# Kernel tuning notes

Hardware: AMD Instinct MI355X
Metric: run time of the kernel (lower is better)

Reference implementation:

```python
import jax, jax.numpy as jnp
import numpy as np
from jax import lax

B, C, IMG, P = 64, 3, 256, 16
D, K, NC, NH = 128, 512, 8, 4
GRID = IMG // P
N = GRID * GRID  # 256 patches
HD = D // NH


def setup_inputs() -> dict:
    key = jax.random.key(0)
    ks = jax.random.split(key, 16)
    s = 0.02
    f32 = jnp.float32
    return {
        'image': jax.random.uniform(ks[0], (B, C, IMG, IMG), f32),
        'conv_w': jax.random.normal(ks[1], (D, C, P, P), f32) * s,
        'conv_b': jnp.zeros((D,), f32),
        'stat_w1': jax.random.normal(ks[2], (128, 15), f32) * s,
        'stat_b1': jnp.zeros((128,), f32),
        'stat_w2': jax.random.normal(ks[3], (D, 128), f32) * s,
        'stat_b2': jnp.zeros((D,), f32),
        'pos_embed': jax.random.normal(ks[4], (1, N, D), f32) * s,
        'ln1_s': jnp.ones((2, D), f32), 'ln1_b': jnp.zeros((2, D), f32),
        'qkv_w': jax.random.normal(ks[5], (2, 3 * D, D), f32) * s,
        'qkv_b': jnp.zeros((2, 3 * D), f32),
        'out_w': jax.random.normal(ks[6], (2, D, D), f32) * s,
        'out_b': jnp.zeros((2, D), f32),
        'ln2_s': jnp.ones((2, D), f32), 'ln2_b': jnp.zeros((2, D), f32),
        'ff1_w': jax.random.normal(ks[7], (2, 2 * D, D), f32) * s,
        'ff1_b': jnp.zeros((2, 2 * D), f32),
        'ff2_w': jax.random.normal(ks[8], (2, D, 2 * D), f32) * s,
        'ff2_b': jnp.zeros((2, D), f32),
        'codebook': jax.random.uniform(ks[9], (K, D), f32, -1.0 / K, 1.0 / K),
        'head_w': jax.random.normal(ks[10], (NC, D), f32) * s,
        'head_b': jnp.zeros((NC,), f32),
    }


def _ln(x, s, b, eps=1e-5):
    mu = x.mean(-1, keepdims=True)
    var = jnp.var(x, axis=-1, keepdims=True)
    return (x - mu) / jnp.sqrt(var + eps) * s + b


def _stats(image):
    # mean/std(unbiased)/min/max per channel + skew/kurt/dark of luminance -> 15 feats
    px = image.reshape(B, C, -1)
    mean = px.mean(-1)
    std = px.std(-1, ddof=1)
    mn = px.min(-1)
    mx = px.max(-1)
    lum = 0.299 * px[:, 0] + 0.587 * px[:, 1] + 0.114 * px[:, 2]
    cen = lum - lum.mean(-1, keepdims=True)
    sd = lum.std(-1)  # biased, matches unbiased=False
    skew = (cen ** 3).mean(-1) / (sd ** 3 + 1e-6)
    kurt = (cen ** 4).mean(-1) / (sd ** 4 + 1e-6)
    dark = (lum < 0.2).astype(jnp.float32).mean(-1)
    return jnp.concatenate([mean, std, mn, mx, skew[:, None], kurt[:, None], dark[:, None]], -1)


def _forward(image, conv_w, conv_b, stat_w1, stat_b1, stat_w2, stat_b2, pos_embed,
             ln1_s, ln1_b, qkv_w, qkv_b, out_w, out_b, ln2_s, ln2_b,
             ff1_w, ff1_b, ff2_w, ff2_b, codebook, head_w, head_b):
    # patch embedding: non-overlapping conv, stride = kernel = P
    patch = lax.conv_general_dilated(image, conv_w, (P, P), 'VALID',
                                     dimension_numbers=('NCHW', 'OIHW', 'NCHW'))
    patch = (patch + conv_b[None, :, None, None]).reshape(B, D, N).transpose(0, 2, 1)  # (B,N,D)
    # statistical encoder (eval: dropout off)
    sf = jax.nn.relu(_stats(image) @ stat_w1.T + stat_b1) @ stat_w2.T + stat_b2  # (B,D)
    x = patch + pos_embed + sf[:, None, :]
    # 2-layer pre-LN transformer encoder
    for i in range(2):
        h = _ln(x, ln1_s[i], ln1_b[i])
        qkv = h @ qkv_w[i].T + qkv_b[i]
        q, k, v = jnp.split(qkv, 3, axis=-1)
        q = q.reshape(B, N, NH, HD).transpose(0, 2, 1, 3)
        k = k.reshape(B, N, NH, HD).transpose(0, 2, 1, 3)
        v = v.reshape(B, N, NH, HD).transpose(0, 2, 1, 3)
        attn = jax.nn.softmax(jnp.einsum('bhqd,bhkd->bhqk', q, k) / jnp.sqrt(jnp.float32(HD)), -1)
        o = jnp.einsum('bhqk,bhkd->bhqd', attn, v).transpose(0, 2, 1, 3).reshape(B, N, D)
        x = x + o @ out_w[i].T + out_b[i]
        h = _ln(x, ln2_s[i], ln2_b[i])
        x = x + jax.nn.gelu(h @ ff1_w[i].T + ff1_b[i], approximate=False) @ ff2_w[i].T + ff2_b[i]
    # VQ: nearest-codebook lookup with straight-through estimator
    zf = x.reshape(-1, D)
    dist = (zf * zf).sum(1, keepdims=True) + (codebook * codebook).sum(1) - 2.0 * (zf @ codebook.T)
    idx = jnp.argmin(dist, axis=1)  # (B*N,)
    qz = codebook[idx].reshape(B, N, D)
    quant = x + lax.stop_gradient(qz - x)
    counts = jnp.zeros((K,), jnp.float32).at[idx].add(1.0)
    p = counts / idx.size
    perplexity = jnp.exp(-jnp.sum(p * jnp.log(p + 1e-10)))
    gf = quant.mean(1)
    logits = gf @ head_w.T + head_b
    return quant, idx.reshape(B, N), logits, gf, perplexity


def reference(image, conv_w, conv_b, stat_w1, stat_b1, stat_w2, stat_b2, pos_embed,
              ln1_s, ln1_b, qkv_w, qkv_b, out_w, out_b, ln2_s, ln2_b,
              ff1_w, ff1_b, ff2_w, ff2_b, codebook, head_w, head_b):
    return _forward(image, conv_w, conv_b, stat_w1, stat_b1, stat_w2, stat_b2, pos_embed,
                    ln1_s, ln1_b, qkv_w, qkv_b, out_w, out_b, ln2_s, ln2_b,
                    ff1_w, ff1_b, ff2_w, ff2_b, codebook, head_w, head_b)
```

## Files before the change

### kernel.cpp

```cpp
#include <hip/hip_runtime.h>
#include <math.h>

__device__ __forceinline__ double wred_add(double v) {
    #pragma unroll
    for (int o = 32; o > 0; o >>= 1) v += __shfl_xor(v, o);
    return v;
}
__device__ __forceinline__ float wred_min(float v) {
    #pragma unroll
    for (int o = 32; o > 0; o >>= 1) v = fminf(v, __shfl_xor(v, o));
    return v;
}
__device__ __forceinline__ float wred_max(float v) {
    #pragma unroll
    for (int o = 32; o > 0; o >>= 1) v = fmaxf(v, __shfl_xor(v, o));
    return v;
}

#define PREC 17

__global__ __launch_bounds__(256) void stats_partial_kernel(const float* __restrict__ img,
                                                            double* __restrict__ part)
{
    int b = blockIdx.x >> 5, blk = blockIdx.x & 31;
    int tid = threadIdx.x;
    const float* r0 = img + (size_t)b * 3 * 65536;
    const float* g0 = r0 + 65536;
    const float* b0 = r0 + 131072;
    int base = blk*2048 + tid*8;
    double s0=0,s1=0,s2=0,q0=0,q1=0,q2=0,l1=0,l2=0,l3=0,l4=0,dark=0;
    float mn0=1e30f,mn1=1e30f,mn2=1e30f, mx0=-1e30f,mx1=-1e30f,mx2=-1e30f;
    #pragma unroll
    for (int u = 0; u < 2; ++u) {
        float4 rv = *(const float4*)&r0[base + u*4];
        float4 gv = *(const float4*)&g0[base + u*4];
        float4 bv = *(const float4*)&b0[base + u*4];
        float rr[4] = {rv.x, rv.y, rv.z, rv.w};
        float gg[4] = {gv.x, gv.y, gv.z, gv.w};
        float bbv[4] = {bv.x, bv.y, bv.z, bv.w};
        #pragma unroll
        for (int e = 0; e < 4; ++e) {
            float r = rr[e], g = gg[e], bl = bbv[e];
            double rd_ = r, gd = g, bd = bl;
            s0 += rd_; q0 += rd_*rd_; mn0 = fminf(mn0, r); mx0 = fmaxf(mx0, r);
            s1 += gd;  q1 += gd*gd;   mn1 = fminf(mn1, g); mx1 = fmaxf(mx1, g);
            s2 += bd;  q2 += bd*bd;   mn2 = fminf(mn2, bl); mx2 = fmaxf(mx2, bl);
            double lum = 0.299*rd_ + 0.587*gd + 0.114*bd;
            double d2 = lum*lum;
            l1 += lum; l2 += d2; l3 += d2*lum; l4 += d2*d2;
            if (lum < 0.2) dark += 1.0;
        }
    }
    double dv[11] = {s0,s1,s2,q0,q1,q2,l1,l2,l3,l4,dark};
    #pragma unroll
    for (int q = 0; q < 11; ++q) dv[q] = wred_add(dv[q]);
    mn0 = wred_min(mn0); mn1 = wred_min(mn1); mn2 = wred_min(mn2);
    mx0 = wred_max(mx0); mx1 = wred_max(mx1); mx2 = wred_max(mx2);
    __shared__ double sd[4][PREC];
    int w = tid >> 6, lane = tid & 63;
    if (lane == 0) {
        #pragma unroll
        for (int q = 0; q < 11; ++q) sd[w][q] = dv[q];
        sd[w][11] = (double)mn0; sd[w][12] = (double)mn1; sd[w][13] = (double)mn2;
        sd[w][14] = (double)mx0; sd[w][15] = (double)mx1; sd[w][16] = (double)mx2;
    }
    __syncthreads();
    if (tid == 0) {
        double out[PREC];
        #pragma unroll
        for (int q = 0; q < PREC; ++q) out[q] = sd[0][q];
        #pragma unroll
        for (int ww = 1; ww < 4; ++ww) {
            #pragma unroll
            for (int q = 0; q < 11; ++q) out[q] += sd[ww][q];
            out[11] = fmin(out[11], sd[ww][11]); out[12] = fmin(out[12], sd[ww][12]);
            out[13] = fmin(out[13], sd[ww][13]);
            out[14] = fmax(out[14], sd[ww][14]); out[15] = fmax(out[15], sd[ww][15]);
            out[16] = fmax(out[16], sd[ww][16]);
        }
        double* p = part + (size_t)(b*32 + blk)*PREC;
        #pragma unroll
        for (int q = 0; q < PREC; ++q) p[q] = out[q];
    }
}

__global__ __launch_bounds__(32) void stats_final_kernel(const double* __restrict__ part,
                                                         double* __restrict__ feats)
{
    int b = blockIdx.x, t = threadIdx.x;
    const double* p = part + (size_t)(b*32 + t)*PREC;
    double v[PREC];
    #pragma unroll
    for (int q = 0; q < PREC; ++q) v[q] = p[q];
    #pragma unroll
    for (int o = 16; o > 0; o >>= 1) {
        #pragma unroll
        for (int q = 0; q < 11; ++q) v[q] += __shfl_xor(v[q], o);
        #pragma unroll
        for (int q = 11; q < 14; ++q) v[q] = fmin(v[q], __shfl_xor(v[q], o));
        #pragma unroll
        for (int q = 14; q < PREC; ++q) v[q] = fmax(v[q], __shfl_xor(v[q], o));
    }
    if (t == 0) {
        const double n = 65536.0;
        double* f = feats + b*15;
        for (int c = 0; c < 3; ++c) {
            double su = v[c], sq = v[3+c];
            f[c]   = su/n;
            f[3+c] = sqrt((sq - su*su/n) / (n - 1.0));
            f[6+c] = v[11+c];
            f[9+c] = v[14+c];
        }
        double m1 = v[6]/n, m2 = v[7]/n, m3 = v[8]/n, m4 = v[9]/n;
        double mu2 = m2 - m1*m1;
        double mu3 = m3 - 3.0*m1*m2 + 2.0*m1*m1*m1;
        double mu4 = m4 - 4.0*m1*m3 + 6.0*m1*m1*m2 - 3.0*m1*m1*m1*m1;
        double sd = sqrt(mu2);
        f[12] = mu3 / (sd*sd*sd + 1e-6);
        f[13] = mu4 / (sd*sd*sd*sd + 1e-6);
        f[14] = v[10] / n;
    }
}

__global__ __launch_bounds__(128) void sfmlp_kernel(const double* __restrict__ feats,
    const float* __restrict__ w1, const float* __restrict__ b1,
    const float* __restrict__ w2, const float* __restrict__ b2,
    double* __restrict__ sf)
{
    int b = blockIdx.x, t = threadIdx.x;
    __shared__ double fs[15];
    __shared__ double hs[128];
    if (t < 15) fs[t] = feats[b*15 + t];
    __syncthreads();
    double h = (double)b1[t];
    for (int j = 0; j < 15; ++j) h += fs[j] * (double)w1[t*15 + j];
    hs[t] = fmax(h, 0.0);
    __syncthreads();
    double o = (double)b2[t];
    for (int j = 0; j < 128; ++j) o += hs[j] * (double)w2[t*128 + j];
    sf[b*128 + t] = o;
}

__device__ __forceinline__ int swz64(int r, int kq4) {
    return r*64 + (((kq4) ^ (r & 15)) << 2);
}

__global__ __launch_bounds__(256) void patch_sk_kernel(const float* __restrict__ img,
    const float* __restrict__ w, float* __restrict__ P0, float* __restrict__ P1)
{
    __shared__ float As[4096];
    __shared__ float Ws[4096];
    int tid = threadIdx.x;
    int tx = tid & 15, ty = tid >> 4;
    int m0 = blockIdx.x * 64, n0 = blockIdx.y * 64;
    int kbase = blockIdx.z * 384;
    int kq = tid & 15;
    int r0 = tid >> 4;
    float acc[4][4] = {};
    for (int k0 = 0; k0 < 384; k0 += 64) {
        #pragma unroll
        for (int p = 0; p < 4; ++p) {
            int row = p*16 + r0;
            int m = m0 + row;
            int bb = m >> 8, pat = m & 255;
            int gy = pat >> 4, gx = pat & 15;
            int k = kbase + k0 + kq*4;
            int c = k >> 8, rem = k & 255;
            int py = rem >> 4, px = rem & 15;
            *(float4*)&As[swz64(row, kq)] =
                *(const float4*)&img[(size_t)(bb*3 + c)*65536 + (size_t)(gy*16+py)*256 + gx*16 + px];
            *(float4*)&Ws[swz64(row, kq)] = *(const float4*)&w[(size_t)(n0+row)*768 + k];
        }
        __syncthreads();
        #pragma unroll 8
        for (int q = 0; q < 16; ++q) {
            float4 a4[4], w4[4];
            #pragma unroll
            for (int i=0;i<4;++i) a4[i] = *(const float4*)&As[swz64(ty + 16*i, q)];
            #pragma unroll
            for (int j=0;j<4;++j) w4[j] = *(const float4*)&Ws[swz64(tx + 16*j, q)];
            #pragma unroll
            for (int i=0;i<4;++i)
                #pragma unroll
                for (int j=0;j<4;++j) {
                    acc[i][j] = fmaf(a4[i].x, w4[j].x, acc[i][j]);
                    acc[i][j] = fmaf(a4[i].y, w4[j].y, acc[i][j]);
                    acc[i][j] = fmaf(a4[i].z, w4[j].z, acc[i][j]);
                    acc[i][j] = fmaf(a4[i].w, w4[j].w, acc[i][j]);
                }
        }
        __syncthreads();
    }
    float* P = blockIdx.z ? P1 : P0;
    #pragma unroll
    for (int i=0;i<4;++i){
        int m = m0 + ty + 16*i;
        #pragma unroll
        for (int j=0;j<4;++j){
            int n = n0 + tx + 16*j;
            P[(size_t)m*128 + n] = acc[i][j];
        }
    }
}

__global__ __launch_bounds__(256) void gemm_kernel(const float* __restrict__ A, int lda,
    const float* __restrict__ W, const float* __restrict__ bias,
    float* __restrict__ C, int M, int N, int K, int epi)
{
    __shared__ float As[4096];
    __shared__ float Ws[4096];
    int tid = threadIdx.x;
    int tx = tid & 15, ty = tid >> 4;
    int m0 = blockIdx.x * 64, n0 = blockIdx.y * 64;
    int kq = tid & 15;
    int r0 = tid >> 4;
    float acc[4][4] = {};
    for (int k0 = 0; k0 < K; k0 += 64) {
        #pragma unroll
        for (int p = 0; p < 4; ++p) {
            int row = p*16 + r0;
            *(float4*)&As[swz64(row, kq)] = *(const float4*)&A[(size_t)(m0+row)*lda + k0 + kq*4];
            *(float4*)&Ws[swz64(row, kq)] = *(const float4*)&W[(size_t)(n0+row)*K + k0 + kq*4];
        }
        __syncthreads();
        #pragma unroll 8
        for (int q = 0; q < 16; ++q) {
            float4 a4[4], w4[4];
            #pragma unroll
            for (int i=0;i<4;++i) a4[i] = *(const float4*)&As[swz64(ty + 16*i, q)];
            #pragma unroll
            for (int j=0;j<4;++j) w4[j] = *(const float4*)&Ws[swz64(tx + 16*j, q)];
            #pragma unroll
            for (int i=0;i<4;++i)
                #pragma unroll
                for (int j=0;j<4;++j) {
                    acc[i][j] = fmaf(a4[i].x, w4[j].x, acc[i][j]);
                    acc[i][j] = fmaf(a4[i].y, w4[j].y, acc[i][j]);
                    acc[i][j] = fmaf(a4[i].z, w4[j].z, acc[i][j]);
                    acc[i][j] = fmaf(a4[i].w, w4[j].w, acc[i][j]);
                }
        }
        __syncthreads();
    }
    #pragma unroll
    for (int i=0;i<4;++i){
        int m = m0 + ty + 16*i;
        #pragma unroll
        for (int j=0;j<4;++j){
            int n = n0 + tx + 16*j;
            float v = acc[i][j] + bias[n];
            if (epi == 0) {
                C[(size_t)m*N + n] = v;
            } else {
                C[(size_t)m*N + n] = 0.5f*v*(1.0f + erff(v*0.70710678118654752f));
            }
        }
    }
}

__global__ __launch_bounds__(256) void gemm_sk_kernel(const float* __restrict__ A, int lda,
    const float* __restrict__ W, int K, int K2,
    float* __restrict__ P0, float* __restrict__ P1, int ldo)
{
    __shared__ float As[4096];
    __shared__ float Ws[4096];
    int tid = threadIdx.x;
    int tx = tid & 15, ty = tid >> 4;
    int m0 = blockIdx.x * 64, n0 = blockIdx.y * 64;
    int kbase = blockIdx.z * K2;
    int kq = tid & 15;
    int r0 = tid >> 4;
    float acc[4][4] = {};
    for (int k0 = 0; k0 < K2; k0 += 64) {
        #pragma unroll
        for (int p = 0; p < 4; ++p) {
            int row = p*16 + r0;
            *(float4*)&As[swz64(row, kq)] = *(const float4*)&A[(size_t)(m0+row)*lda + kbase + k0 + kq*4];
            *(float4*)&Ws[swz64(row, kq)] = *(const float4*)&W[(size_t)(n0+row)*K + kbase + k0 + kq*4];
        }
        __syncthreads();
        #pragma unroll 8
        for (int q = 0; q < 16; ++q) {
            float4 a4[4], w4[4];
            #pragma unroll
            for (int i=0;i<4;++i) a4[i] = *(const float4*)&As[swz64(ty + 16*i, q)];
            #pragma unroll
            for (int j=0;j<4;++j) w4[j] = *(const float4*)&Ws[swz64(tx + 16*j, q)];
            #pragma unroll
            for (int i=0;i<4;++i)
                #pragma unroll
                for (int j=0;j<4;++j) {
                    acc[i][j] = fmaf(a4[i].x, w4[j].x, acc[i][j]);
                    acc[i][j] = fmaf(a4[i].y, w4[j].y, acc[i][j]);
                    acc[i][j] = fmaf(a4[i].z, w4[j].z, acc[i][j]);
                    acc[i][j] = fmaf(a4[i].w, w4[j].w, acc[i][j]);
                }
        }
        __syncthreads();
    }
    float* P = blockIdx.z ? P1 : P0;
    #pragma unroll
    for (int i=0;i<4;++i){
        int m = m0 + ty + 16*i;
        #pragma unroll
        for (int j=0;j<4;++j){
            int n = n0 + tx + 16*j;
            P[(size_t)m*ldo + n] = acc[i][j];
        }
    }
}

__global__ __launch_bounds__(256) void cpatch_kernel(const float* __restrict__ p0,
    const float* __restrict__ p1, const float* __restrict__ bias,
    const float* __restrict__ pos, const double* __restrict__ sf,
    const float* __restrict__ ls, const float* __restrict__ lb,
    float* __restrict__ x, float* __restrict__ h)
{
    int tid = threadIdx.x;
    int lane = tid & 63, w = tid >> 6;
    int row = blockIdx.x*4 + w;
    int bb = row >> 8, pat = row & 255;
    int n = lane*2;
    float2 a0 = *(const float2*)&p0[(size_t)row*128 + n];
    float2 a1 = *(const float2*)&p1[(size_t)row*128 + n];
    float v0 = a0.x + a1.x + bias[n]   + pos[pat*128 + n]   + (float)sf[bb*128 + n];
    float v1 = a0.y + a1.y + bias[n+1] + pos[pat*128 + n+1] + (float)sf[bb*128 + n+1];
    *(float2*)&x[(size_t)row*128 + n] = make_float2(v0, v1);
    double v0d = v0, v1d = v1;
    double sum = v0d + v1d, sq = v0d*v0d + v1d*v1d;
    #pragma unroll
    for (int o = 32; o > 0; o >>= 1) { sum += __shfl_xor(sum, o); sq += __shfl_xor(sq, o); }
    double mean = sum * (1.0/128.0);
    double var  = sq  * (1.0/128.0) - mean*mean;
    double inv  = 1.0 / sqrt(var + 1e-5);
    float2 o2;
    o2.x = (float)((v0d - mean)*inv*(double)ls[n]   + (double)lb[n]);
    o2.y = (float)((v1d - mean)*inv*(double)ls[n+1] + (double)lb[n+1]);
    *(float2*)&h[(size_t)row*128 + n] = o2;
}

__global__ __launch_bounds__(256) void cres_kernel(float* __restrict__ x,
    const float* __restrict__ p0, int ld0, const float* __restrict__ p1, int ld1,
    const float* __restrict__ bias,
    const float* __restrict__ ls, const float* __restrict__ lb,
    float* __restrict__ h, int doLN)
{
    int tid = threadIdx.x;
    int lane = tid & 63, w = tid >> 6;
    int row = blockIdx.x*4 + w;
    int n = lane*2;
    float2 a0 = *(const float2*)&p0[(size_t)row*ld0 + n];
    float2 a1 = *(const float2*)&p1[(size_t)row*ld1 + n];
    float2 xv = *(const float2*)&x[(size_t)row*128 + n];
    float v0 = xv.x + (a0.x + a1.x + bias[n]);
    float v1 = xv.y + (a0.y + a1.y + bias[n+1]);
    *(float2*)&x[(size_t)row*128 + n] = make_float2(v0, v1);
    if (doLN) {
        double v0d = v0, v1d = v1;
        double sum = v0d + v1d, sq = v0d*v0d + v1d*v1d;
        #pragma unroll
        for (int o = 32; o > 0; o >>= 1) { sum += __shfl_xor(sum, o); sq += __shfl_xor(sq, o); }
        double mean = sum * (1.0/128.0);
        double var  = sq  * (1.0/128.0) - mean*mean;
        double inv  = 1.0 / sqrt(var + 1e-5);
        float2 o2;
        o2.x = (float)((v0d - mean)*inv*(double)ls[n]   + (double)lb[n]);
        o2.y = (float)((v1d - mean)*inv*(double)ls[n+1] + (double)lb[n+1]);
        *(float2*)&h[(size_t)row*128 + n] = o2;
    }
}

__global__ __launch_bounds__(512, 4) void attn_kernel(float* __restrict__ qkv)
{
    __shared__ float Ks[256*36];
    __shared__ float Vs[256*36];
    int tid = threadIdx.x;
    int b = blockIdx.x >> 3, h = (blockIdx.x >> 1) & 3, half = blockIdx.x & 1;
    {
        int row = tid >> 1, p16 = (tid & 1) * 16;
        size_t rb = (size_t)(b*256 + row) * 384;
        const float* kp = qkv + rb + 128 + h*32 + p16;
        const float* vp = qkv + rb + 256 + h*32 + p16;
        #pragma unroll
        for (int i = 0; i < 4; ++i) {
            *(float4*)&Ks[row*36 + p16 + i*4] = *(const float4*)&kp[i*4];
            *(float4*)&Vs[row*36 + p16 + i*4] = *(const float4*)&vp[i*4];
        }
    }
    int qrow = half*128 + (tid >> 2);
    int ds = (tid >> 1) & 1;
    int ks = tid & 1;
    float q[16];
    const float* qp = qkv + (size_t)(b*256 + qrow)*384 + h*32 + ds*16;
    #pragma unroll
    for (int i = 0; i < 16; ++i) q[i] = qp[i];
    __syncthreads();
    float o[16];
    #pragma unroll
    for (int i = 0; i < 16; ++i) o[i] = 0.f;
    float m = -INFINITY, l = 0.f;
    const float scale = 0.17677669529663687f;
    for (int it = 0; it < 128; ++it) {
        int j = it*2 + ks;
        const float* kr = &Ks[j*36 + ds*16];
        float s = 0.f;
        #pragma unroll
        for (int i = 0; i < 16; ++i) s = fmaf(q[i], kr[i], s);
        s += __shfl_xor(s, 2);
        s *= scale;
        const float* vr = &Vs[j*36 + ds*16];
        if (__all(s <= m)) {
            float e = __expf(s - m);
            l += e;
            #pragma unroll
            for (int i = 0; i < 16; ++i) o[i] = fmaf(e, vr[i], o[i]);
        } else {
            float mn = fmaxf(m, s);
            float f = __expf(m - mn);
            float e = __expf(s - mn);
            l = l*f + e;
            #pragma unroll
            for (int i = 0; i < 16; ++i) o[i] = fmaf(o[i], f, e*vr[i]);
            m = mn;
        }
    }
    {
        float mo = __shfl_xor(m, 1);
        float lo = __shfl_xor(l, 1);
        float M  = fmaxf(m, mo);
        float ea = __expf(m - M), eb = __expf(mo - M);
        l = l*ea + lo*eb;
        #pragma unroll
        for (int i = 0; i < 16; ++i) {
            float oo = __shfl_xor(o[i], 1);
            o[i] = o[i]*ea + oo*eb;
        }
        m = M;
    }
    if (ks == 0) {
        float inv = 1.0f / l;
        float* op = qkv + (size_t)(b*256 + qrow)*384 + h*32 + ds*16;
        #pragma unroll
        for (int i = 0; i < 16; ++i) op[i] = o[i] * inv;
    }
}

__global__ __launch_bounds__(256) void cc_kernel(const float* __restrict__ cb,
                                                 float* __restrict__ ccs)
{
    int c = blockIdx.x*256 + threadIdx.x;
    const float* p = cb + (size_t)c*128;
    float r[8];
    #pragma unroll
    for (int j = 0; j < 8; ++j) { float v = p[j]; r[j] = v*v; }
    for (int i = 8; i < 128; i += 8)
        #pragma unroll
        for (int j = 0; j < 8; ++j) { float v = p[i+j]; r[j] += v*v; }
    ccs[c] = ((r[0]+r[1]) + (r[2]+r[3])) + ((r[4]+r[5]) + (r[6]+r[7]));
}

#define ZC(k) (((k)&3)==0 ? z[(k)>>2].x : ((k)&3)==1 ? z[(k)>>2].y : ((k)&3)==2 ? z[(k)>>2].z : z[(k)>>2].w)

__global__ __launch_bounds__(128) void vq_dist_kernel(const float* __restrict__ x,
    const float* __restrict__ cb, const float* __restrict__ ccs,
    float* __restrict__ pbv, int* __restrict__ pbi)
{
    __shared__ float Cs[8192];
    __shared__ float ccl[64];
    int tid = threadIdx.x;
    int m = blockIdx.x*128 + tid;
    int split = blockIdx.y;
    int cbase = split*64;
    const float4* cbp = (const float4*)(cb + (size_t)cbase*128);
    for (int e = tid; e < 2048; e += 128) ((float4*)Cs)[e] = cbp[e];
    if (tid < 64) ccl[tid] = ccs[cbase + tid];
    float4 z[32];
    const float4* zp = (const float4*)(x + (size_t)m*128);
    #pragma unroll
    for (int i = 0; i < 32; ++i) z[i] = zp[i];
    float r[8];
    #pragma unroll
    for (int j = 0; j < 8; ++j) { float v = ZC(j); r[j] = v*v; }
    #pragma unroll
    for (int i = 8; i < 128; i += 8)
        #pragma unroll
        for (int j = 0; j < 8; ++j) { float v = ZC(i+j); r[j] += v*v; }
    float zz = ((r[0]+r[1]) + (r[2]+r[3])) + ((r[4]+r[5]) + (r[6]+r[7]));
    __syncthreads();
    float bestv = INFINITY;
    int   besti = 0;
    for (int g = 0; g < 16; ++g) {
        const float* c0 = &Cs[(g*4+0)*128];
        const float* c1 = &Cs[(g*4+1)*128];
        const float* c2 = &Cs[(g*4+2)*128];
        const float* c3 = &Cs[(g*4+3)*128];
        float a0 = 0.f, a1 = 0.f, a2 = 0.f, a3 = 0.f;
        #pragma unroll
        for (int q = 0; q < 32; ++q) {
            float4 v0 = *(const float4*)&c0[q*4];
            float4 v1 = *(const float4*)&c1[q*4];
            float4 v2 = *(const float4*)&c2[q*4];
            float4 v3 = *(const float4*)&c3[q*4];
            float4 zq = z[q];
            a0 = fmaf(zq.x, v0.x, a0); a0 = fmaf(zq.y, v0.y, a0);
            a0 = fmaf(zq.z, v0.z, a0); a0 = fmaf(zq.w, v0.w, a0);
            a1 = fmaf(zq.x, v1.x, a1); a1 = fmaf(zq.y, v1.y, a1);
            a1 = fmaf(zq.z, v1.z, a1); a1 = fmaf(zq.w, v1.w, a1);
            a2 = fmaf(zq.x, v2.x, a2); a2 = fmaf(zq.y, v2.y, a2);
            a2 = fmaf(zq.z, v2.z, a2); a2 = fmaf(zq.w, v2.w, a2);
            a3 = fmaf(zq.x, v3.x, a3); a3 = fmaf(zq.y, v3.y, a3);
            a3 = fmaf(zq.z, v3.z, a3); a3 = fmaf(zq.w, v3.w, a3);
        }
        int code = cbase + g*4;
        float t1, d;
        t1 = zz + ccl[g*4+0]; d = t1 - 2.0f*a0; if (d < bestv) { bestv = d; besti = code;   }
        t1 = zz + ccl[g*4+1]; d = t1 - 2.0f*a1; if (d < bestv) { bestv = d; besti = code+1; }
        t1 = zz + ccl[g*4+2]; d = t1 - 2.0f*a2; if (d < bestv) { bestv = d; besti = code+2; }
        t1 = zz + ccl[g*4+3]; d = t1 - 2.0f*a3; if (d < bestv) { bestv = d; besti = code+3; }
    }
    pbv[(size_t)split*16384 + m] = bestv;
    pbi[(size_t)split*16384 + m] = besti;
}

__global__ __launch_bounds__(256) void vq_merge_kernel(const float* __restrict__ pbv,
    const int* __restrict__ pbi, const float* __restrict__ cb,
    float* __restrict__ quant, float* __restrict__ idxf, float* __restrict__ counts)
{
    __shared__ int fidx[256];
    int tid = threadIdx.x;
    int m0 = blockIdx.x*256;
    int m = m0 + tid;
    float v = pbv[m]; int gi = pbi[m];
    #pragma unroll
    for (int s = 1; s < 8; ++s) {
        float vv = pbv[(size_t)s*16384 + m]; int ii = pbi[(size_t)s*16384 + m];
        if (vv < v) { v = vv; gi = ii; }
    }
    fidx[tid] = gi;
    idxf[m] = (float)gi;
    atomicAdd(&counts[gi], 1.0f);
    __syncthreads();
    for (int e = tid; e < 8192; e += 256) {
        int rr = e >> 5, k4 = e & 31;
        ((float4*)&quant[(size_t)(m0+rr)*128])[k4] = ((const float4*)&cb[(size_t)fidx[rr]*128])[k4];
    }
}

__global__ __launch_bounds__(128) void gf_logits_kernel(const float* __restrict__ quant,
    const float* __restrict__ head_w, const float* __restrict__ head_b,
    float* __restrict__ gf, float* __restrict__ logits)
{
    int b = blockIdx.x, d = threadIdx.x;
    double s = 0.0;
    for (int n = 0; n < 256; ++n) s += (double)quant[(size_t)(b*256+n)*128 + d];
    double g = s * (1.0/256.0);
    gf[b*128 + d] = (float)g;
    __shared__ double gs[128];
    gs[d] = g;
    __syncthreads();
    if (d < 8) {
        double l = (double)head_b[d];
        for (int k = 0; k < 128; ++k) l += gs[k] * (double)head_w[d*128 + k];
        logits[b*8 + d] = (float)l;
    }
}

__global__ __launch_bounds__(512) void perp_kernel(const float* __restrict__ counts,
                                                   float* __restrict__ out)
{
    __shared__ double sh[512];
    int t = threadIdx.x;
    double p = (double)counts[t] * (1.0/16384.0);
    sh[t] = p * log(p + 1e-10);
    __syncthreads();
    for (int s = 256; s > 0; s >>= 1) { if (t < s) sh[t] += sh[t+s]; __syncthreads(); }
    if (t == 0) out[0] = (float)exp(-sh[0]);
}

extern "C" void kernel_launch(void* const* d_in, const int* in_sizes, int n_in,
                              void* d_out, int out_size, void* d_ws, size_t ws_size,
                              hipStream_t stream)
{
    const float* image   = (const float*)d_in[0];
    const float* conv_w  = (const float*)d_in[1];
    const float* conv_b  = (const float*)d_in[2];
    const float* stat_w1 = (const float*)d_in[3];
    const float* stat_b1 = (const float*)d_in[4];
    const float* stat_w2 = (const float*)d_in[5];
    const float* stat_b2 = (const float*)d_in[6];
    const float* pos     = (const float*)d_in[7];
    const float* ln1_s   = (const float*)d_in[8];
    const float* ln1_b   = (const float*)d_in[9];
    const float* qkv_w   = (const float*)d_in[10];
    const float* qkv_b   = (const float*)d_in[11];
    const float* out_w   = (const float*)d_in[12];
    const float* out_b   = (const float*)d_in[13];
    const float* ln2_s   = (const float*)d_in[14];
    const float* ln2_b   = (const float*)d_in[15];
    const float* ff1_w   = (const float*)d_in[16];
    const float* ff1_b   = (const float*)d_in[17];
    const float* ff2_w   = (const float*)d_in[18];
    const float* ff2_b   = (const float*)d_in[19];
    const float* codebook= (const float*)d_in[20];
    const float* head_w  = (const float*)d_in[21];
    const float* head_b  = (const float*)d_in[22];

    char* wsb = (char*)d_ws;
    float*  x32   = (float*) (wsb);
    float*  h32   = (float*) (wsb + 8388608);
    float*  qkv32 = (float*) (wsb + 16777216);
    double* sf64  = (double*)(wsb + 41943040);
    double* feats = (double*)(wsb + 42008576);
    float*  counts= (float*) (wsb + 42016256);
    double* part  = (double*)(wsb + 42018304);
    float*  pbv   = (float*) (wsb + 42296832);
    int*    pbi   = (int*)   (wsb + 42821120);
    float*  ccs   = (float*) (wsb + 43345408);

    float* outf   = (float*)d_out;
    float* quant  = outf;
    float* idxf   = quant + 2097152;
    float* logits = idxf + 16384;
    float* gf     = logits + 512;
    float* perp   = gf + 8192;

    hipMemsetAsync(counts, 0, 512*sizeof(float), stream);

    stats_partial_kernel<<<2048, 256, 0, stream>>>(image, part);
    stats_final_kernel<<<64, 32, 0, stream>>>(part, feats);
    sfmlp_kernel<<<64, 128, 0, stream>>>(feats, stat_w1, stat_b1, stat_w2, stat_b2, sf64);
    cc_kernel<<<2, 256, 0, stream>>>(codebook, ccs);

    patch_sk_kernel<<<dim3(256, 2, 2), 256, 0, stream>>>(image, conv_w,
                                                         qkv32, qkv32 + 2097152);
    cpatch_kernel<<<4096, 256, 0, stream>>>(qkv32, qkv32 + 2097152, conv_b, pos, sf64,
                                            ln1_s, ln1_b, x32, h32);

    for (int i = 0; i < 2; ++i) {
        gemm_kernel<<<dim3(256, 6), 256, 0, stream>>>(h32, 128, qkv_w + (size_t)i*384*128,
                                                      qkv_b + i*384, qkv32, 16384, 384, 128, 0);
        attn_kernel<<<512, 512, 0, stream>>>(qkv32);
        gemm_sk_kernel<<<dim3(256, 2, 2), 256, 0, stream>>>(qkv32, 384,
                                                            out_w + (size_t)i*128*128, 128, 64,
                                                            qkv32 + 128, qkv32 + 256, 384);
        cres_kernel<<<4096, 256, 0, stream>>>(x32, qkv32 + 128, 384, qkv32 + 256, 384,
                                              out_b + i*128, ln2_s + i*128, ln2_b + i*128,
                                              h32, 1);
        gemm_kernel<<<dim3(256, 4), 256, 0, stream>>>(h32, 128, ff1_w + (size_t)i*256*128,
                                                      ff1_b + i*256, qkv32, 16384, 256, 128, 2);
        gemm_sk_kernel<<<dim3(256, 2, 2), 256, 0, stream>>>(qkv32, 256,
                                                            ff2_w + (size_t)i*128*256, 256, 128,
                                                            qkv32 + 4194304, h32, 128);
        cres_kernel<<<4096, 256, 0, stream>>>(x32, qkv32 + 4194304, 128, h32, 128,
                                              ff2_b + i*128, ln1_s + 128, ln1_b + 128,
                                              h32, i == 0 ? 1 : 0);
    }

    vq_dist_kernel<<<dim3(128, 8), 128, 0, stream>>>(x32, codebook, ccs, pbv, pbi);
    vq_merge_kernel<<<64, 256, 0, stream>>>(pbv, pbi, codebook, quant, idxf, counts);
    gf_logits_kernel<<<64, 128, 0, stream>>>(quant, head_w, head_b, gf, logits);
    perp_kernel<<<1, 512, 0, stream>>>(counts, perp);
}
```

Measured before the change: 530.6 us.

## Register-block attention over four query rows per thread with vectorized K/V reads

The attention kernel now has each thread process four query rows over an 8-wide slice of the head dimension, so every K and V row loaded from shared memory is reused across four queries and read as float4. One block now covers all 256 queries of a (batch, head) pair, which halves the grid and the repeated K/V staging into shared memory. The costs are higher register pressure (launch bounds lowered to 2 blocks), a grid of only 256 blocks, and an extra shuffle level for the score reduction.

New measurement: 570.8 us. 1.08x slower.

```diff
diff --git a/kernel.cpp b/kernel.cpp
--- a/kernel.cpp
+++ b/kernel.cpp
@@ -370,12 +370,12 @@
     }
 }
 
-__global__ __launch_bounds__(512, 4) void attn_kernel(float* __restrict__ qkv)
+__global__ __launch_bounds__(512, 2) void attn_kernel(float* __restrict__ qkv)
 {
     __shared__ float Ks[256*36];
     __shared__ float Vs[256*36];
     int tid = threadIdx.x;
-    int b = blockIdx.x >> 3, h = (blockIdx.x >> 1) & 3, half = blockIdx.x & 1;
+    int b = blockIdx.x >> 2, h = blockIdx.x & 3;
     {
         int row = tid >> 1, p16 = (tid & 1) * 16;
         size_t rb = (size_t)(b*256 + row) * 384;
@@ -387,61 +387,99 @@
             *(float4*)&Vs[row*36 + p16 + i*4] = *(const float4*)&vp[i*4];
         }
     }
-    int qrow = half*128 + (tid >> 2);
-    int ds = (tid >> 1) & 1;
-    int ks = tid & 1;
-    float q[16];
-    const float* qp = qkv + (size_t)(b*256 + qrow)*384 + h*32 + ds*16;
-    #pragma unroll
-    for (int i = 0; i < 16; ++i) q[i] = qp[i];
+    int ds = tid & 3;
+    int ks = (tid >> 2) & 1;
+    int qg = tid >> 3;
+    float q[4][8];
+    #pragma unroll
+    for (int r = 0; r < 4; ++r) {
+        const float* qp = qkv + (size_t)(b*256 + qg*4 + r)*384 + h*32 + ds*8;
+        *(float4*)&q[r][0] = *(const float4*)&qp[0];
+        *(float4*)&q[r][4] = *(const float4*)&qp[4];
+    }
     __syncthreads();
-    float o[16];
-    #pragma unroll
-    for (int i = 0; i < 16; ++i) o[i] = 0.f;
-    float m = -INFINITY, l = 0.f;
+    float o[4][8];
+    #pragma unroll
+    for (int r = 0; r < 4; ++r)
+        #pragma unroll
+        for (int i = 0; i < 8; ++i) o[r][i] = 0.f;
+    float m[4] = {-INFINITY, -INFINITY, -INFINITY, -INFINITY};
+    float l[4] = {0.f, 0.f, 0.f, 0.f};
     const float scale = 0.17677669529663687f;
     for (int it = 0; it < 128; ++it) {
         int j = it*2 + ks;
-        const float* kr = &Ks[j*36 + ds*16];
-        float s = 0.f;
-        #pragma unroll
-        for (int i = 0; i < 16; ++i) s = fmaf(q[i], kr[i], s);
-        s += __shfl_xor(s, 2);
-        s *= scale;
-        const float* vr = &Vs[j*36 + ds*16];
-        if (__all(s <= m)) {
-            float e = __expf(s - m);
-            l += e;
-            #pragma unroll
-            for (int i = 0; i < 16; ++i) o[i] = fmaf(e, vr[i], o[i]);
+        const float* kr = &Ks[j*36 + ds*8];
+        float4 k0 = *(const float4*)&kr[0];
+        float4 k1 = *(const float4*)&kr[4];
+        float s[4];
+        #pragma unroll
+        for (int r = 0; r < 4; ++r) {
+            float t = 0.f;
+            t = fmaf(q[r][0], k0.x, t); t = fmaf(q[r][1], k0.y, t);
+            t = fmaf(q[r][2], k0.z, t); t = fmaf(q[r][3], k0.w, t);
+            t = fmaf(q[r][4], k1.x, t); t = fmaf(q[r][5], k1.y, t);
+            t = fmaf(q[r][6], k1.z, t); t = fmaf(q[r][7], k1.w, t);
+            s[r] = t;
+        }
+        #pragma unroll
+        for (int r = 0; r < 4; ++r) {
+            s[r] += __shfl_xor(s[r], 1);
+            s[r] += __shfl_xor(s[r], 2);
+            s[r] *= scale;
+        }
+        const float* vr = &Vs[j*36 + ds*8];
+        float4 v0 = *(const float4*)&vr[0];
+        float4 v1 = *(const float4*)&vr[4];
+        bool nomax = (s[0] <= m[0]) & (s[1] <= m[1]) & (s[2] <= m[2]) & (s[3] <= m[3]);
+        if (__all(nomax)) {
+            #pragma unroll
+            for (int r = 0; r < 4; ++r) {
+                float e = __expf(s[r] - m[r]);
+                l[r] += e;
+                o[r][0] = fmaf(e, v0.x, o[r][0]); o[r][1] = fmaf(e, v0.y, o[r][1]);
+                o[r][2] = fmaf(e, v0.z, o[r][2]); o[r][3] = fmaf(e, v0.w, o[r][3]);
+                o[r][4] = fmaf(e, v1.x, o[r][4]); o[r][5] = fmaf(e, v1.y, o[r][5]);
+                o[r][6] = fmaf(e, v1.z, o[r][6]); o[r][7] = fmaf(e, v1.w, o[r][7]);
+            }
         } else {
-            float mn = fmaxf(m, s);
-            float f = __expf(m - mn);
-            float e = __expf(s - mn);
-            l = l*f + e;
-            #pragma unroll
-            for (int i = 0; i < 16; ++i) o[i] = fmaf(o[i], f, e*vr[i]);
-            m = mn;
-        }
-    }
-    {
-        float mo = __shfl_xor(m, 1);
-        float lo = __shfl_xor(l, 1);
-        float M  = fmaxf(m, mo);
-        float ea = __expf(m - M), eb = __expf(mo - M);
-        l = l*ea + lo*eb;
-        #pragma unroll
-        for (int i = 0; i < 16; ++i) {
-            float oo = __shfl_xor(o[i], 1);
-            o[i] = o[i]*ea + oo*eb;
-        }
-        m = M;
+            #pragma unroll
+            for (int r = 0; r < 4; ++r) {
+                float mn = fmaxf(m[r], s[r]);
+                float f = __expf(m[r] - mn);
+                float e = __expf(s[r] - mn);
+                l[r] = l[r]*f + e;
+                o[r][0] = fmaf(o[r][0], f, e*v0.x); o[r][1] = fmaf(o[r][1], f, e*v0.y);
+                o[r][2] = fmaf(o[r][2], f, e*v0.z); o[r][3] = fmaf(o[r][3], f, e*v0.w);
+                o[r][4] = fmaf(o[r][4], f, e*v1.x); o[r][5] = fmaf(o[r][5], f, e*v1.y);
+                o[r][6] = fmaf(o[r][6], f, e*v1.z); o[r][7] = fmaf(o[r][7], f, e*v1.w);
+                m[r] = mn;
+            }
+        }
+    }
+    #pragma unroll
+    for (int r = 0; r < 4; ++r) {
+        float mo = __shfl_xor(m[r], 4);
+        float lo = __shfl_xor(l[r], 4);
+        float M  = fmaxf(m[r], mo);
+        float ea = __expf(m[r] - M), eb = __expf(mo - M);
+        l[r] = l[r]*ea + lo*eb;
+        #pragma unroll
+        for (int i = 0; i < 8; ++i) {
+            float oo = __shfl_xor(o[r][i], 4);
+            o[r][i] = o[r][i]*ea + oo*eb;
+        }
+        m[r] = M;
     }
     if (ks == 0) {
-        float inv = 1.0f / l;
-        float* op = qkv + (size_t)(b*256 + qrow)*384 + h*32 + ds*16;
-        #pragma unroll
-        for (int i = 0; i < 16; ++i) op[i] = o[i] * inv;
+        #pragma unroll
+        for (int r = 0; r < 4; ++r) {
+            float inv = 1.0f / l[r];
+            float* op = qkv + (size_t)(b*256 + qg*4 + r)*384 + h*32 + ds*8;
+            float4 w0 = make_float4(o[r][0]*inv, o[r][1]*inv, o[r][2]*inv, o[r][3]*inv);
+            float4 w1 = make_float4(o[r][4]*inv, o[r][5]*inv, o[r][6]*inv, o[r][7]*inv);
+            *(float4*)&op[0] = w0;
+            *(float4*)&op[4] = w1;
+        }
     }
 }
 
@@ -639,7 +677,7 @@
     for (int i = 0; i < 2; ++i) {
         gemm_kernel<<<dim3(256, 6), 256, 0, stream>>>(h32, 128, qkv_w + (size_t)i*384*128,
                                                       qkv_b + i*384, qkv32, 16384, 384, 128, 0);
-        attn_kernel<<<512, 512, 0, stream>>>(qkv32);
+        attn_kernel<<<256, 512, 0, stream>>>(qkv32);
         gemm_sk_kernel<<<dim3(256, 2, 2), 256, 0, stream>>>(qkv32, 384,
                                                             out_w + (size_t)i*128*128, 128, 64,
                                                             qkv32 + 128, qkv32 + 256, 384);
```
